# Kernel tuning notes

Hardware: AMD Instinct MI355X
Metric: run time of the kernel (lower is better)

## Reference

```python
import jax, jax.numpy as jnp
import numpy as np
from jax.scipy.ndimage import map_coordinates

N_ANGLES = 120


def _radon3d(vol):
    """Faithful port of radon_transform_3d_pet(axis=2 path) + radon_torch_2d.

    vol: [1, 1, D, H, W].  Slices are vol[:, :, :, d] (dim 3), stacked over
    range(W) -- valid because H == W here.  Returns sinogram stack [S, A, L].
    """
    B, C, D, H, W = vol.shape  # B = C = 1
    imgs = jnp.moveaxis(vol[0, 0], 1, 0)  # [S=H, D, W]; slice s = vol[0,0,:,s,:]

    L = int(np.ceil(np.sqrt(D * D + W * W)))  # padded square canvas
    top = (L - D) // 2   # pad_h // 2
    left = (L - W) // 2  # pad_w // 2

    angles = jnp.linspace(0.0, 120.0, N_ANGLES) * (jnp.pi / 180.0)
    cos_t, sin_t = jnp.cos(angles), jnp.sin(angles)

    # affine_grid with align_corners=True over an L x L output
    lin = jnp.linspace(-1.0, 1.0, L)
    xg, yg = jnp.meshgrid(lin, lin)  # [L, L]; xg varies along columns
    x_in = cos_t[:, None, None] * xg - sin_t[:, None, None] * yg  # [A, L, L]
    y_in = sin_t[:, None, None] * xg + cos_t[:, None, None] * yg
    # unnormalize (align_corners=True) and shift into the UNpadded image frame;
    # zeros in the pad region == map_coordinates mode='constant', cval=0
    ix = (x_in + 1.0) * 0.5 * (L - 1) - left  # column coord into [D, W] image
    iy = (y_in + 1.0) * 0.5 * (L - 1) - top   # row coord

    def sample(im):  # im: [D, W] -> rotated canvases [A, L, L]
        return map_coordinates(im, [iy, ix], order=1, mode='constant', cval=0.0)

    rot = jax.vmap(sample)(imgs)        # [S, A, L, L]
    return rot.sum(axis=2)              # sum over rows -> [S, A, L]


def setup_inputs() -> dict:
    key = jax.random.key(0)
    k1, k2 = jax.random.split(key)
    shape = (1, 1, 64, 64, 64)
    out = jax.random.uniform(k1, shape, dtype=jnp.float32)
    gt = jax.random.uniform(k2, shape, dtype=jnp.float32)
    return {"out": out, "gt": gt}


def reference(out, gt):
    so = _radon3d(out)  # [S, A, L]
    sg = _radon3d(gt)
    # sum over slices of per-slice mean L1 (matches the Python loop of F.l1_loss)
    return jnp.abs(so - sg).mean(axis=(1, 2)).sum()
```

## Files before the change

### kernel.cpp

```cpp
#include <hip/hip_runtime.h>

#define DD 64
#define NA 120
#define LL 91
#define PS 67
#define PSTR 69
#define NCELL (PS * PSTR)
#define NSL 8
#define NANG 4
#define JT 96
#define NTHR (NANG * JT)
#define NSP (64 / NSL)
#define NAP (NA / NANG)
#define NBLKS (NSP * NAP)

typedef float f32x2 __attribute__((ext_vector_type(2)));

static __device__ __forceinline__ void sample8(
    const uint2* __restrict__ P, float fi, float sn, float c,
    float bx1, float by1, float* __restrict__ acc)
{
    const float xs = fminf(fmaxf(fmaf(-fi, sn, bx1), 0.0f), 65.0f);
    const float ys = fminf(fmaxf(fmaf( fi, c,  by1), 0.0f), 65.0f);
    const int ix = (int)xs;
    const int iy = (int)ys;
    const float wx = xs - (float)ix;
    const float wy = ys - (float)iy;
    const float ux = 1.f - wx, uy = 1.f - wy;
    const float w00 = ux * uy, w01 = wx * uy;
    const float w10 = ux * wy, w11 = wx * wy;
    const int ci = iy * PSTR + ix;
    const uint2 q00 = P[ci],        q01 = P[ci + 1];
    const uint2 q10 = P[ci + PSTR], q11 = P[ci + PSTR + 1];
    f32x2 v;
    v = __builtin_amdgcn_cvt_pk_f32_fp8(q00.x, false); acc[0] = fmaf(w00, v.x, acc[0]); acc[1] = fmaf(w00, v.y, acc[1]);
    v = __builtin_amdgcn_cvt_pk_f32_fp8(q00.x, true);  acc[2] = fmaf(w00, v.x, acc[2]); acc[3] = fmaf(w00, v.y, acc[3]);
    v = __builtin_amdgcn_cvt_pk_f32_fp8(q00.y, false); acc[4] = fmaf(w00, v.x, acc[4]); acc[5] = fmaf(w00, v.y, acc[5]);
    v = __builtin_amdgcn_cvt_pk_f32_fp8(q00.y, true);  acc[6] = fmaf(w00, v.x, acc[6]); acc[7] = fmaf(w00, v.y, acc[7]);
    v = __builtin_amdgcn_cvt_pk_f32_fp8(q01.x, false); acc[0] = fmaf(w01, v.x, acc[0]); acc[1] = fmaf(w01, v.y, acc[1]);
    v = __builtin_amdgcn_cvt_pk_f32_fp8(q01.x, true);  acc[2] = fmaf(w01, v.x, acc[2]); acc[3] = fmaf(w01, v.y, acc[3]);
    v = __builtin_amdgcn_cvt_pk_f32_fp8(q01.y, false); acc[4] = fmaf(w01, v.x, acc[4]); acc[5] = fmaf(w01, v.y, acc[5]);
    v = __builtin_amdgcn_cvt_pk_f32_fp8(q01.y, true);  acc[6] = fmaf(w01, v.x, acc[6]); acc[7] = fmaf(w01, v.y, acc[7]);
    v = __builtin_amdgcn_cvt_pk_f32_fp8(q10.x, false); acc[0] = fmaf(w10, v.x, acc[0]); acc[1] = fmaf(w10, v.y, acc[1]);
    v = __builtin_amdgcn_cvt_pk_f32_fp8(q10.x, true);  acc[2] = fmaf(w10, v.x, acc[2]); acc[3] = fmaf(w10, v.y, acc[3]);
    v = __builtin_amdgcn_cvt_pk_f32_fp8(q10.y, false); acc[4] = fmaf(w10, v.x, acc[4]); acc[5] = fmaf(w10, v.y, acc[5]);
    v = __builtin_amdgcn_cvt_pk_f32_fp8(q10.y, true);  acc[6] = fmaf(w10, v.x, acc[6]); acc[7] = fmaf(w10, v.y, acc[7]);
    v = __builtin_amdgcn_cvt_pk_f32_fp8(q11.x, false); acc[0] = fmaf(w11, v.x, acc[0]); acc[1] = fmaf(w11, v.y, acc[1]);
    v = __builtin_amdgcn_cvt_pk_f32_fp8(q11.x, true);  acc[2] = fmaf(w11, v.x, acc[2]); acc[3] = fmaf(w11, v.y, acc[3]);
    v = __builtin_amdgcn_cvt_pk_f32_fp8(q11.y, false); acc[4] = fmaf(w11, v.x, acc[4]); acc[5] = fmaf(w11, v.y, acc[5]);
    v = __builtin_amdgcn_cvt_pk_f32_fp8(q11.y, true);  acc[6] = fmaf(w11, v.x, acc[6]); acc[7] = fmaf(w11, v.y, acc[7]);
}

__global__ __launch_bounds__(NTHR, 2) void radon_loss_kernel(
    const float* __restrict__ vout, const float* __restrict__ vgt,
    float* __restrict__ out)
{
    __shared__ uint2 P[NCELL];
    __shared__ float wsum[NTHR / 64];

    const int bid = blockIdx.x;
    const int sp = bid / NAP;
    const int ap = bid - sp * NAP;
    const int s0 = sp * NSL;
    const int t = threadIdx.x;

    for (int idx = t; idx < NCELL; idx += NTHR)
        P[idx] = make_uint2(0u, 0u);
    __syncthreads();

    for (int idx = t; idx < DD * DD; idx += NTHR) {
        const int d = idx >> 6, w = idx & 63;
        const int g = d * 4096 + s0 * 64 + w;
        float df[NSL];
        #pragma unroll
        for (int k = 0; k < NSL; ++k)
            df[k] = vout[g + 64 * k] - vgt[g + 64 * k];
        int p0 = 0, p1 = 0;
        p0 = __builtin_amdgcn_cvt_pk_fp8_f32(df[0], df[1], p0, false);
        p0 = __builtin_amdgcn_cvt_pk_fp8_f32(df[2], df[3], p0, true);
        p1 = __builtin_amdgcn_cvt_pk_fp8_f32(df[4], df[5], p1, false);
        p1 = __builtin_amdgcn_cvt_pk_fp8_f32(df[6], df[7], p1, true);
        P[(d + 1) * PSTR + (w + 1)] = make_uint2((unsigned)p0, (unsigned)p1);
    }
    __syncthreads();

    const int ja = t / JT;
    const int j  = t - ja * JT;
    const int a  = ap * NANG + ja;
    const float theta = (float)a * (float)(3.14159265358979323846 * 120.0 / 119.0 / 180.0);
    const float c = cosf(theta), sn = sinf(theta);

    float val = 0.f;
    if (j < LL) {
        const float linj = fmaf((float)j, 2.0f / 90.0f, -1.0f);
        const float bx1 = fmaf(c,  linj, 1.0f) * 45.0f - 12.0f + 45.0f * sn;
        const float by1 = fmaf(sn, linj, 1.0f) * 45.0f - 12.0f - 45.0f * c;
        float accA[8] = {0.f, 0.f, 0.f, 0.f, 0.f, 0.f, 0.f, 0.f};
        float accB[8] = {0.f, 0.f, 0.f, 0.f, 0.f, 0.f, 0.f, 0.f};
        #pragma unroll 3
        for (int i = 0; i < 45; ++i) {
            sample8(P, (float)i,        sn, c, bx1, by1, accA);
            sample8(P, (float)(i + 46), sn, c, bx1, by1, accB);
        }
        sample8(P, 45.0f, sn, c, bx1, by1, accA);
        #pragma unroll
        for (int k = 0; k < 8; ++k)
            val += fabsf(accA[k] + accB[k]);
    }

    #pragma unroll
    for (int off = 32; off > 0; off >>= 1)
        val += __shfl_down(val, off);
    const int wave = t >> 6, lane = t & 63;
    if (lane == 0) wsum[wave] = val;
    __syncthreads();
    if (t == 0) {
        float v = 0.f;
        #pragma unroll
        for (int wv = 0; wv < NTHR / 64; ++wv) v += wsum[wv];
        atomicAdd(out, v * (1.0f / (float)(NA * LL)));
    }
}

extern "C" void kernel_launch(void* const* d_in, const int* in_sizes, int n_in,
                              void* d_out, int out_size, void* d_ws, size_t ws_size,
                              hipStream_t stream) {
    const float* vout = (const float*)d_in[0];
    const float* vgt  = (const float*)d_in[1];
    float* out = (float*)d_out;

    hipMemsetAsync(out, 0, sizeof(float), stream);
    radon_loss_kernel<<<NBLKS, NTHR, 0, stream>>>(vout, vgt, out);
}
```

Baseline: 81.46 us.

## Split into canvas-build kernel and global-memory projection kernel with paired-column cells

Moves canvas construction into a separate kernel that writes a padded fp8 difference canvas to workspace memory, storing each cell together with its right neighbour as a uint4. The projection kernel then reads two 16-byte global loads per sample instead of four LDS loads. Each block now handles one angle and eight slices, with the ray split into two halves and combined through shared memory. This removes the per-block redundant canvas build and LDS staging, at the cost of an extra launch, a global round trip, and cache-dependent gather loads.

```diff
diff --git a/kernel.cpp b/kernel.cpp
--- a/kernel.cpp
+++ b/kernel.cpp
@@ -6,106 +6,127 @@
 #define PS 67
 #define PSTR 69
 #define NCELL (PS * PSTR)
+#define NCELLP 4624
 #define NSL 8
-#define NANG 4
+#define NGRP (64 / NSL)
 #define JT 96
-#define NTHR (NANG * JT)
-#define NSP (64 / NSL)
-#define NAP (NA / NANG)
-#define NBLKS (NSP * NAP)
+#define PTHR (2 * JT)
+#define PBLKS (NGRP * NA)
+#define BLD_BLK ((NCELLP + 255) / 256)
 
 typedef float f32x2 __attribute__((ext_vector_type(2)));
 
-static __device__ __forceinline__ void sample8(
-    const uint2* __restrict__ P, float fi, float sn, float c,
-    float bx1, float by1, float* __restrict__ acc)
+__global__ __launch_bounds__(256) void build_canvas_kernel(
+    const float* __restrict__ vout, const float* __restrict__ vgt,
+    uint4* __restrict__ C)
 {
-    const float xs = fminf(fmaxf(fmaf(-fi, sn, bx1), 0.0f), 65.0f);
-    const float ys = fminf(fmaxf(fmaf( fi, c,  by1), 0.0f), 65.0f);
-    const int ix = (int)xs;
-    const int iy = (int)ys;
-    const float wx = xs - (float)ix;
-    const float wy = ys - (float)iy;
-    const float ux = 1.f - wx, uy = 1.f - wy;
-    const float w00 = ux * uy, w01 = wx * uy;
-    const float w10 = ux * wy, w11 = wx * wy;
-    const int ci = iy * PSTR + ix;
-    const uint2 q00 = P[ci],        q01 = P[ci + 1];
-    const uint2 q10 = P[ci + PSTR], q11 = P[ci + PSTR + 1];
-    f32x2 v;
-    v = __builtin_amdgcn_cvt_pk_f32_fp8(q00.x, false); acc[0] = fmaf(w00, v.x, acc[0]); acc[1] = fmaf(w00, v.y, acc[1]);
-    v = __builtin_amdgcn_cvt_pk_f32_fp8(q00.x, true);  acc[2] = fmaf(w00, v.x, acc[2]); acc[3] = fmaf(w00, v.y, acc[3]);
-    v = __builtin_amdgcn_cvt_pk_f32_fp8(q00.y, false); acc[4] = fmaf(w00, v.x, acc[4]); acc[5] = fmaf(w00, v.y, acc[5]);
-    v = __builtin_amdgcn_cvt_pk_f32_fp8(q00.y, true);  acc[6] = fmaf(w00, v.x, acc[6]); acc[7] = fmaf(w00, v.y, acc[7]);
-    v = __builtin_amdgcn_cvt_pk_f32_fp8(q01.x, false); acc[0] = fmaf(w01, v.x, acc[0]); acc[1] = fmaf(w01, v.y, acc[1]);
-    v = __builtin_amdgcn_cvt_pk_f32_fp8(q01.x, true);  acc[2] = fmaf(w01, v.x, acc[2]); acc[3] = fmaf(w01, v.y, acc[3]);
-    v = __builtin_amdgcn_cvt_pk_f32_fp8(q01.y, false); acc[4] = fmaf(w01, v.x, acc[4]); acc[5] = fmaf(w01, v.y, acc[5]);
-    v = __builtin_amdgcn_cvt_pk_f32_fp8(q01.y, true);  acc[6] = fmaf(w01, v.x, acc[6]); acc[7] = fmaf(w01, v.y, acc[7]);
-    v = __builtin_amdgcn_cvt_pk_f32_fp8(q10.x, false); acc[0] = fmaf(w10, v.x, acc[0]); acc[1] = fmaf(w10, v.y, acc[1]);
-    v = __builtin_amdgcn_cvt_pk_f32_fp8(q10.x, true);  acc[2] = fmaf(w10, v.x, acc[2]); acc[3] = fmaf(w10, v.y, acc[3]);
-    v = __builtin_amdgcn_cvt_pk_f32_fp8(q10.y, false); acc[4] = fmaf(w10, v.x, acc[4]); acc[5] = fmaf(w10, v.y, acc[5]);
-    v = __builtin_amdgcn_cvt_pk_f32_fp8(q10.y, true);  acc[6] = fmaf(w10, v.x, acc[6]); acc[7] = fmaf(w10, v.y, acc[7]);
-    v = __builtin_amdgcn_cvt_pk_f32_fp8(q11.x, false); acc[0] = fmaf(w11, v.x, acc[0]); acc[1] = fmaf(w11, v.y, acc[1]);
-    v = __builtin_amdgcn_cvt_pk_f32_fp8(q11.x, true);  acc[2] = fmaf(w11, v.x, acc[2]); acc[3] = fmaf(w11, v.y, acc[3]);
-    v = __builtin_amdgcn_cvt_pk_f32_fp8(q11.y, false); acc[4] = fmaf(w11, v.x, acc[4]); acc[5] = fmaf(w11, v.y, acc[5]);
-    v = __builtin_amdgcn_cvt_pk_f32_fp8(q11.y, true);  acc[6] = fmaf(w11, v.x, acc[6]); acc[7] = fmaf(w11, v.y, acc[7]);
+    const int bid = blockIdx.x;
+    const int g = bid / BLD_BLK;
+    const int cell = (bid - g * BLD_BLK) * 256 + threadIdx.x;
+    if (cell >= NCELL) return;
+    const int y = cell / PSTR;
+    const int x = cell - y * PSTR;
+    const int d = y - 1;
+    const int w0 = x - 1, w1 = x;
+    uint4 val = make_uint4(0u, 0u, 0u, 0u);
+    if ((unsigned)d < DD) {
+        const int rowbase = d * 4096 + g * NSL * 64;
+        if ((unsigned)w0 < DD) {
+            int p0 = 0, p1 = 0;
+            float df[NSL];
+            #pragma unroll
+            for (int k = 0; k < NSL; ++k)
+                df[k] = vout[rowbase + 64 * k + w0] - vgt[rowbase + 64 * k + w0];
+            p0 = __builtin_amdgcn_cvt_pk_fp8_f32(df[0], df[1], p0, false);
+            p0 = __builtin_amdgcn_cvt_pk_fp8_f32(df[2], df[3], p0, true);
+            p1 = __builtin_amdgcn_cvt_pk_fp8_f32(df[4], df[5], p1, false);
+            p1 = __builtin_amdgcn_cvt_pk_fp8_f32(df[6], df[7], p1, true);
+            val.x = (unsigned)p0; val.y = (unsigned)p1;
+        }
+        if ((unsigned)w1 < DD) {
+            int p0 = 0, p1 = 0;
+            float df[NSL];
+            #pragma unroll
+            for (int k = 0; k < NSL; ++k)
+                df[k] = vout[rowbase + 64 * k + w1] - vgt[rowbase + 64 * k + w1];
+            p0 = __builtin_amdgcn_cvt_pk_fp8_f32(df[0], df[1], p0, false);
+            p0 = __builtin_amdgcn_cvt_pk_fp8_f32(df[2], df[3], p0, true);
+            p1 = __builtin_amdgcn_cvt_pk_fp8_f32(df[4], df[5], p1, false);
+            p1 = __builtin_amdgcn_cvt_pk_fp8_f32(df[6], df[7], p1, true);
+            val.z = (unsigned)p0; val.w = (unsigned)p1;
+        }
+    }
+    C[g * NCELLP + cell] = val;
 }
 
-__global__ __launch_bounds__(NTHR, 2) void radon_loss_kernel(
-    const float* __restrict__ vout, const float* __restrict__ vgt,
-    float* __restrict__ out)
+__global__ __launch_bounds__(PTHR) void radon_proj_kernel(
+    const uint4* __restrict__ C, float* __restrict__ out)
 {
-    __shared__ uint2 P[NCELL];
-    __shared__ float wsum[NTHR / 64];
+    __shared__ float colsum[LL][NSL];
+    __shared__ float wsum[PTHR / 64];
 
     const int bid = blockIdx.x;
-    const int sp = bid / NAP;
-    const int ap = bid - sp * NAP;
-    const int s0 = sp * NSL;
+    const int g = bid / NA;
+    const int a = bid - g * NA;
     const int t = threadIdx.x;
+    const int half = t / JT;
+    const int j = t - half * JT;
 
-    for (int idx = t; idx < NCELL; idx += NTHR)
-        P[idx] = make_uint2(0u, 0u);
-    __syncthreads();
-
-    for (int idx = t; idx < DD * DD; idx += NTHR) {
-        const int d = idx >> 6, w = idx & 63;
-        const int g = d * 4096 + s0 * 64 + w;
-        float df[NSL];
-        #pragma unroll
-        for (int k = 0; k < NSL; ++k)
-            df[k] = vout[g + 64 * k] - vgt[g + 64 * k];
-        int p0 = 0, p1 = 0;
-        p0 = __builtin_amdgcn_cvt_pk_fp8_f32(df[0], df[1], p0, false);
-        p0 = __builtin_amdgcn_cvt_pk_fp8_f32(df[2], df[3], p0, true);
-        p1 = __builtin_amdgcn_cvt_pk_fp8_f32(df[4], df[5], p1, false);
-        p1 = __builtin_amdgcn_cvt_pk_fp8_f32(df[6], df[7], p1, true);
-        P[(d + 1) * PSTR + (w + 1)] = make_uint2((unsigned)p0, (unsigned)p1);
-    }
-    __syncthreads();
-
-    const int ja = t / JT;
-    const int j  = t - ja * JT;
-    const int a  = ap * NANG + ja;
     const float theta = (float)a * (float)(3.14159265358979323846 * 120.0 / 119.0 / 180.0);
     const float c = cosf(theta), sn = sinf(theta);
 
-    float val = 0.f;
+    float acc[NSL] = {0.f, 0.f, 0.f, 0.f, 0.f, 0.f, 0.f, 0.f};
     if (j < LL) {
         const float linj = fmaf((float)j, 2.0f / 90.0f, -1.0f);
         const float bx1 = fmaf(c,  linj, 1.0f) * 45.0f - 12.0f + 45.0f * sn;
         const float by1 = fmaf(sn, linj, 1.0f) * 45.0f - 12.0f - 45.0f * c;
-        float accA[8] = {0.f, 0.f, 0.f, 0.f, 0.f, 0.f, 0.f, 0.f};
-        float accB[8] = {0.f, 0.f, 0.f, 0.f, 0.f, 0.f, 0.f, 0.f};
+        const uint4* __restrict__ Cg = C + g * NCELLP;
+        const int i0 = half ? 46 : 0;
+        const int i1 = half ? LL : 46;
         #pragma unroll 3
-        for (int i = 0; i < 45; ++i) {
-            sample8(P, (float)i,        sn, c, bx1, by1, accA);
-            sample8(P, (float)(i + 46), sn, c, bx1, by1, accB);
+        for (int i = i0; i < i1; ++i) {
+            const float xs = fminf(fmaxf(fmaf(-(float)i, sn, bx1), 0.0f), 65.0f);
+            const float ys = fminf(fmaxf(fmaf( (float)i, c,  by1), 0.0f), 65.0f);
+            const int ix = (int)xs;
+            const int iy = (int)ys;
+            const float wx = xs - (float)ix;
+            const float wy = ys - (float)iy;
+            const float ux = 1.f - wx, uy = 1.f - wy;
+            const float w00 = ux * uy, w01 = wx * uy;
+            const float w10 = ux * wy, w11 = wx * wy;
+            const int ci = iy * PSTR + ix;
+            const uint4 q0 = Cg[ci];
+            const uint4 q1 = Cg[ci + PSTR];
+            f32x2 v;
+            v = __builtin_amdgcn_cvt_pk_f32_fp8(q0.x, false); acc[0] = fmaf(w00, v.x, acc[0]); acc[1] = fmaf(w00, v.y, acc[1]);
+            v = __builtin_amdgcn_cvt_pk_f32_fp8(q0.x, true);  acc[2] = fmaf(w00, v.x, acc[2]); acc[3] = fmaf(w00, v.y, acc[3]);
+            v = __builtin_amdgcn_cvt_pk_f32_fp8(q0.y, false); acc[4] = fmaf(w00, v.x, acc[4]); acc[5] = fmaf(w00, v.y, acc[5]);
+            v = __builtin_amdgcn_cvt_pk_f32_fp8(q0.y, true);  acc[6] = fmaf(w00, v.x, acc[6]); acc[7] = fmaf(w00, v.y, acc[7]);
+            v = __builtin_amdgcn_cvt_pk_f32_fp8(q0.z, false); acc[0] = fmaf(w01, v.x, acc[0]); acc[1] = fmaf(w01, v.y, acc[1]);
+            v = __builtin_amdgcn_cvt_pk_f32_fp8(q0.z, true);  acc[2] = fmaf(w01, v.x, acc[2]); acc[3] = fmaf(w01, v.y, acc[3]);
+            v = __builtin_amdgcn_cvt_pk_f32_fp8(q0.w, false); acc[4] = fmaf(w01, v.x, acc[4]); acc[5] = fmaf(w01, v.y, acc[5]);
+            v = __builtin_amdgcn_cvt_pk_f32_fp8(q0.w, true);  acc[6] = fmaf(w01, v.x, acc[6]); acc[7] = fmaf(w01, v.y, acc[7]);
+            v = __builtin_amdgcn_cvt_pk_f32_fp8(q1.x, false); acc[0] = fmaf(w10, v.x, acc[0]); acc[1] = fmaf(w10, v.y, acc[1]);
+            v = __builtin_amdgcn_cvt_pk_f32_fp8(q1.x, true);  acc[2] = fmaf(w10, v.x, acc[2]); acc[3] = fmaf(w10, v.y, acc[3]);
+            v = __builtin_amdgcn_cvt_pk_f32_fp8(q1.y, false); acc[4] = fmaf(w10, v.x, acc[4]); acc[5] = fmaf(w10, v.y, acc[5]);
+            v = __builtin_amdgcn_cvt_pk_f32_fp8(q1.y, true);  acc[6] = fmaf(w10, v.x, acc[6]); acc[7] = fmaf(w10, v.y, acc[7]);
+            v = __builtin_amdgcn_cvt_pk_f32_fp8(q1.z, false); acc[0] = fmaf(w11, v.x, acc[0]); acc[1] = fmaf(w11, v.y, acc[1]);
+            v = __builtin_amdgcn_cvt_pk_f32_fp8(q1.z, true);  acc[2] = fmaf(w11, v.x, acc[2]); acc[3] = fmaf(w11, v.y, acc[3]);
+            v = __builtin_amdgcn_cvt_pk_f32_fp8(q1.w, false); acc[4] = fmaf(w11, v.x, acc[4]); acc[5] = fmaf(w11, v.y, acc[5]);
+            v = __builtin_amdgcn_cvt_pk_f32_fp8(q1.w, true);  acc[6] = fmaf(w11, v.x, acc[6]); acc[7] = fmaf(w11, v.y, acc[7]);
         }
-        sample8(P, 45.0f, sn, c, bx1, by1, accA);
+    }
+
+    if (half == 0 && j < LL) {
         #pragma unroll
-        for (int k = 0; k < 8; ++k)
-            val += fabsf(accA[k] + accB[k]);
+        for (int k = 0; k < NSL; ++k) colsum[j][k] = acc[k];
+    }
+    __syncthreads();
+    float val = 0.f;
+    if (half == 1 && j < LL) {
+        #pragma unroll
+        for (int k = 0; k < NSL; ++k)
+            val += fabsf(colsum[j][k] + acc[k]);
     }
 
     #pragma unroll
@@ -117,7 +138,7 @@
     if (t == 0) {
         float v = 0.f;
         #pragma unroll
-        for (int wv = 0; wv < NTHR / 64; ++wv) v += wsum[wv];
+        for (int wv = 0; wv < PTHR / 64; ++wv) v += wsum[wv];
         atomicAdd(out, v * (1.0f / (float)(NA * LL)));
     }
 }
@@ -128,7 +149,9 @@
     const float* vout = (const float*)d_in[0];
     const float* vgt  = (const float*)d_in[1];
     float* out = (float*)d_out;
+    uint4* canvas = (uint4*)d_ws;
 
     hipMemsetAsync(out, 0, sizeof(float), stream);
-    radon_loss_kernel<<<NBLKS, NTHR, 0, stream>>>(vout, vgt, out);
+    build_canvas_kernel<<<NGRP * BLD_BLK, 256, 0, stream>>>(vout, vgt, canvas);
+    radon_proj_kernel<<<PBLKS, PTHR, 0, stream>>>(canvas, out);
 }
```

Result: slower. 83.80 us (+2.9%).
